# Performance work log

Measured on AMD Instinct MI355X. Metric: run time of the kernel, lower is better.

## Reference

```python
import jax, jax.numpy as jnp
import numpy as np

SHAPE = (192, 192, 192)


def _trilinear_sample(img, z, y, x):
    # img: [B,C,D,H,W]; z,y,x: [B,D,H,W] absolute voxel coords (align_corners=True,
    # zero padding outside the volume, matching F.grid_sample defaults in vroc).
    B, C, D, H, W = img.shape
    imgf = img.reshape(B, C, -1)
    z0 = jnp.floor(z); y0 = jnp.floor(y); x0 = jnp.floor(x)
    wz = z - z0; wy = y - y0; wx = x - x0
    z0i = z0.astype(jnp.int32); y0i = y0.astype(jnp.int32); x0i = x0.astype(jnp.int32)
    z1i = z0i + 1; y1i = y0i + 1; x1i = x0i + 1

    def gather(iz, iy, ix):
        valid = ((iz >= 0) & (iz < D) & (iy >= 0) & (iy < H) & (ix >= 0) & (ix < W))
        lin = ((jnp.clip(iz, 0, D - 1) * H + jnp.clip(iy, 0, H - 1)) * W
               + jnp.clip(ix, 0, W - 1)).reshape(B, 1, -1)
        v = jnp.take_along_axis(imgf, jnp.broadcast_to(lin, (B, C, D * H * W)), axis=2)
        return v.reshape(B, C, D, H, W) * valid.reshape(B, 1, D, H, W).astype(img.dtype)

    def w(a, b, c):
        return (a * b * c)[:, None]  # [B,1,D,H,W]

    out = (gather(z0i, y0i, x0i) * w(1 - wz, 1 - wy, 1 - wx)
           + gather(z0i, y0i, x1i) * w(1 - wz, 1 - wy, wx)
           + gather(z0i, y1i, x0i) * w(1 - wz, wy, 1 - wx)
           + gather(z0i, y1i, x1i) * w(1 - wz, wy, wx)
           + gather(z1i, y0i, x0i) * w(wz, 1 - wy, 1 - wx)
           + gather(z1i, y0i, x1i) * w(wz, 1 - wy, wx)
           + gather(z1i, y1i, x0i) * w(wz, wy, 1 - wx)
           + gather(z1i, y1i, x1i) * w(wz, wy, wx))
    return out


def _warp(moving_image, vector_field):
    # SpatialTransformer: identity grid + displacement (voxel units), trilinear sample.
    B, C, D, H, W = moving_image.shape
    dt = moving_image.dtype
    gz, gy, gx = jnp.meshgrid(jnp.arange(D, dtype=dt), jnp.arange(H, dtype=dt),
                              jnp.arange(W, dtype=dt), indexing='ij')
    z = gz[None] + vector_field[:, 0]
    y = gy[None] + vector_field[:, 1]
    x = gx[None] + vector_field[:, 2]
    return _trilinear_sample(moving_image, z, y, x)


def setup_inputs() -> dict:
    key = jax.random.key(0)
    k1, k2, k3, k4 = jax.random.split(key, 4)
    D, H, W = SHAPE
    moving_image = jax.random.normal(k1, (1, 1, D, H, W), dtype=jnp.float32)
    vector_field = jax.random.normal(k2, (1, 3, D, H, W), dtype=jnp.float32) * 3.0
    fixed_image = jax.random.normal(k3, (1, 1, D, H, W), dtype=jnp.float32)
    fixed_image_mask = jax.random.randint(k4, (1, 1, D, H, W), 0, 2).astype(bool)
    return {"moving_image": moving_image, "vector_field": vector_field,
            "fixed_image": fixed_image, "fixed_image_mask": fixed_image_mask}


def reference(moving_image, vector_field, fixed_image, fixed_image_mask):
    warped = _warp(moving_image, vector_field)
    m = fixed_image_mask.astype(warped.dtype)
    sq = (warped - fixed_image) ** 2
    # F.mse_loss(warped[mask], fixed[mask]) == mean of squared diff over masked voxels
    return jnp.sum(sq * m) / jnp.maximum(jnp.sum(m), 1.0)
```

## Files before the change

### kernel.cpp

```cpp
#include <hip/hip_runtime.h>
#include <hip/hip_fp16.h>

#define DD 192
#define HH 192
#define WW 192
#define NVOX (DD * HH * WW)

#define RSX 32
#define RSY 33
#define RSZ 33
#define ROWD 16
#define SLABD (RSY * ROWD)
#define RTOTH (RSX * RSY * RSZ)
#define RTOTD (RTOTH / 2)
#define NCHUNK (RTOTH / 8)
#define CHSLAB (RSY * 4)
#define NT 1024
#define GRID 256
#define QCAP 512

#define AS1 __attribute__((address_space(1)))
#define AS3 __attribute__((address_space(3)))

__global__ __launch_bounds__(256) void conv_fp16(
    const float4* __restrict__ in, int4* __restrict__ out)
{
    const int i = blockIdx.x * 256 + threadIdx.x;
    const float4 a = in[2 * i];
    const float4 b = in[2 * i + 1];
    __half2 h0 = __floats2half2_rn(a.x, a.y);
    __half2 h1 = __floats2half2_rn(a.z, a.w);
    __half2 h2 = __floats2half2_rn(b.x, b.y);
    __half2 h3 = __floats2half2_rn(b.z, b.w);
    int4 o;
    o.x = *(int*)&h0; o.y = *(int*)&h1; o.z = *(int*)&h2; o.w = *(int*)&h3;
    out[i] = o;
}

struct Streams { float4 dz, dy, dx, f; int4 m; };

__device__ __forceinline__ void tile_coords(int n, int& tx, int& ty, int& tz) {
    tx = n / 144;
    const int r = n - tx * 144;
    ty = r / 12;
    tz = r - ty * 12;
}

__device__ __forceinline__ void stage_tile(
    const ushort* __restrict__ movh, const ushort* __restrict__ zbuf,
    uint* sbufd, int x_lo, int y_lo, int z_lo, int tid)
{
    ushort* sbuf = (ushort*)sbufd;
    #pragma unroll
    for (int i = 0; i < 5; ++i) {
        const int q = tid + i * NT;
        if (q < NCHUNK) {
            const int rz = q / CHSLAB;
            const int rem = q - rz * CHSLAB;
            const int ry = rem >> 2;
            const int k  = rem & 3;
            const int gz = z_lo + rz, gy = y_lo + ry, gx = x_lo + 8 * k;
            const bool valid = ((unsigned)gz < DD) & ((unsigned)gy < HH) &
                               ((unsigned)gx < WW);
            const ushort* src = valid ? (movh + ((gz * HH + gy) * WW + gx)) : zbuf;
            const int qb = i * NT + (tid & ~63);
            __builtin_amdgcn_global_load_lds((AS1 void*)src,
                                             (AS3 void*)(sbuf + 8 * qb), 16, 0, 0);
        }
    }
}

__device__ __forceinline__ Streams prefetch_streams(
    const float* __restrict__ vf, const float* __restrict__ fix,
    const int* __restrict__ mask, int base)
{
    Streams s;
    s.dz = *(const float4*)(vf + base);
    s.dy = *(const float4*)(vf + NVOX + base);
    s.dx = *(const float4*)(vf + 2 * NVOX + base);
    s.f  = *(const float4*)(fix + base);
    s.m  = *(const int4*)(mask + base);
    return s;
}

__global__ __launch_bounds__(NT) void warp_mse_persist(
    const ushort* __restrict__ movh,
    const float* __restrict__ mov,
    const float* __restrict__ vf,
    const float* __restrict__ fix,
    const int* __restrict__ mask,
    const ushort* __restrict__ zbuf,
    float* __restrict__ acc,
    float* __restrict__ out)
{
    __shared__ uint sbufd[2][RTOTD];
    __shared__ float s_sq[16], s_cnt[16];
    __shared__ unsigned qn[2];
    __shared__ uint  qp[QCAP];
    __shared__ float4 qw[QCAP];

    const int tid = threadIdx.x;
    const int b = blockIdx.x;
    const int start = b * 6 + min(b, 192);
    const int cnt_t = 6 + (b < 192 ? 1 : 0);

    const int lxg = (tid & 3) * 4;
    const int ly  = (tid >> 2) & 15;
    const int lz  = tid >> 6;

    float sq = 0.0f, cntm = 0.0f;

    if (tid < 2) qn[tid] = 0;
    int tx, ty, tz;
    tile_coords(start, tx, ty, tz);
    stage_tile(movh, zbuf, sbufd[0], tx * 16 - 8, ty * 16 - 8, tz * 16 - 8, tid);
    Streams S0 = prefetch_streams(vf, fix, mask,
        ((tz * 16 + lz) * HH + ty * 16 + ly) * WW + tx * 16 + lxg);
    __syncthreads();

    for (int k = 0; k < cnt_t; ++k) {
        const int cur = k & 1;
        Streams S1 = S0;
        if (k + 1 < cnt_t) {
            int nx, ny, nz;
            tile_coords(start + k + 1, nx, ny, nz);
            stage_tile(movh, zbuf, sbufd[cur ^ 1],
                       nx * 16 - 8, ny * 16 - 8, nz * 16 - 8, tid);
            S1 = prefetch_streams(vf, fix, mask,
                ((nz * 16 + lz) * HH + ny * 16 + ly) * WW + nx * 16 + lxg);
        }

        int cx, cy, cz;
        tile_coords(start + k, cx, cy, cz);
        const int x_lo = cx * 16 - 8, y_lo = cy * 16 - 8, z_lo = cz * 16 - 8;
        const int gz = cz * 16 + lz, gy = cy * 16 + ly, gx0 = cx * 16 + lxg;
        const uint* sdw = sbufd[cur];

        auto proc = [&](float dz, float dy, float dx, float f, int m, int j) {
            const float z = (float)gz + dz, y = (float)gy + dy,
                        x = (float)(gx0 + j) + dx;
            const float z0f = floorf(z), y0f = floorf(y), x0f = floorf(x);
            const float wz = z - z0f, wy = y - y0f, wx = x - x0f;
            const int z0 = (int)z0f, y0 = (int)y0f, x0 = (int)x0f;
            const int z0l = z0 - z_lo, y0l = y0 - y_lo, x0l = x0 - x_lo;
            const bool inbox = ((unsigned)z0l < RSZ - 1) &
                               ((unsigned)y0l < RSY - 1) &
                               ((unsigned)x0l < RSX - 1);
            if (inbox) {
                const int o = z0l * SLABD + y0l * ROWD + (x0l >> 1);
                const bool odd = (x0l & 1) != 0;
                const uint a00 = sdw[o];
                const uint b00 = sdw[o + 1];
                const uint a01 = sdw[o + ROWD];
                const uint b01 = sdw[o + ROWD + 1];
                const uint a10 = sdw[o + SLABD];
                const uint b10 = sdw[o + SLABD + 1];
                const uint a11 = sdw[o + SLABD + ROWD];
                const uint b11 = sdw[o + SLABD + ROWD + 1];
                float v000, v001, v010, v011, v100, v101, v110, v111;
                auto pr = [&](uint A, uint B, float& l, float& r) {
                    const float2 fa = __half22float2(*(const __half2*)&A);
                    const float fb = __low2float(*(const __half2*)&B);
                    l = odd ? fa.y : fa.x;
                    r = odd ? fb   : fa.y;
                };
                pr(a00, b00, v000, v001);
                pr(a01, b01, v010, v011);
                pr(a10, b10, v100, v101);
                pr(a11, b11, v110, v111);
                const float c00 = v000 + (v001 - v000) * wx;
                const float c01 = v010 + (v011 - v010) * wx;
                const float c10 = v100 + (v101 - v100) * wx;
                const float c11 = v110 + (v111 - v110) * wx;
                const float c0 = c00 + (c01 - c00) * wy;
                const float c1 = c10 + (c11 - c10) * wy;
                const float warped = c0 + (c1 - c0) * wz;
                const float mm = (m != 0) ? 1.0f : 0.0f;
                const float diff = warped - f;
                sq += diff * diff * mm;
                cntm += mm;
            } else {
                const uint slot = atomicAdd(&qn[cur], 1u);
                if (slot < QCAP) {
                    const int px = min(max(x0, -5), 196) + 8;
                    const int py = min(max(y0, -5), 196) + 8;
                    const int pz = min(max(z0, -5), 196) + 8;
                    qp[slot] = (uint)px | ((uint)py << 8) | ((uint)pz << 16) |
                               ((m != 0) ? 0x80000000u : 0u);
                    qw[slot] = make_float4(wx, wy, wz, f);
                } else {
                    const int z1 = z0 + 1, y1 = y0 + 1, x1 = x0 + 1;
                    const bool zi0 = (unsigned)z0 < DD, zi1 = (unsigned)z1 < DD;
                    const bool yi0 = (unsigned)y0 < HH, yi1 = (unsigned)y1 < HH;
                    const bool xi0 = (unsigned)x0 < WW, xi1 = (unsigned)x1 < WW;
                    auto ld = [&](int iz, int iy, int ix, bool ok) -> float {
                        return ok ? mov[(iz * HH + iy) * WW + ix] : 0.0f;
                    };
                    const float v000 = ld(z0, y0, x0, zi0 & yi0 & xi0);
                    const float v001 = ld(z0, y0, x1, zi0 & yi0 & xi1);
                    const float v010 = ld(z0, y1, x0, zi0 & yi1 & xi0);
                    const float v011 = ld(z0, y1, x1, zi0 & yi1 & xi1);
                    const float v100 = ld(z1, y0, x0, zi1 & yi0 & xi0);
                    const float v101 = ld(z1, y0, x1, zi1 & yi0 & xi1);
                    const float v110 = ld(z1, y1, x0, zi1 & yi1 & xi0);
                    const float v111 = ld(z1, y1, x1, zi1 & yi1 & xi1);
                    const float c00 = v000 + (v001 - v000) * wx;
                    const float c01 = v010 + (v011 - v010) * wx;
                    const float c10 = v100 + (v101 - v100) * wx;
                    const float c11 = v110 + (v111 - v110) * wx;
                    const float c0 = c00 + (c01 - c00) * wy;
                    const float c1 = c10 + (c11 - c10) * wy;
                    const float warped = c0 + (c1 - c0) * wz;
                    const float mm = (m != 0) ? 1.0f : 0.0f;
                    const float diff = warped - f;
                    sq += diff * diff * mm;
                    cntm += mm;
                }
            }
        };
        proc(S0.dz.x, S0.dy.x, S0.dx.x, S0.f.x, S0.m.x, 0);
        proc(S0.dz.y, S0.dy.y, S0.dx.y, S0.f.y, S0.m.y, 1);
        proc(S0.dz.z, S0.dy.z, S0.dx.z, S0.f.z, S0.m.z, 2);
        proc(S0.dz.w, S0.dy.w, S0.dx.w, S0.f.w, S0.m.w, 3);

        __syncthreads();

        const uint qcount = min(qn[cur], (uint)QCAP);
        if (tid == 0) qn[cur ^ 1] = 0;
        for (uint i = tid; i < qcount; i += NT) {
            const uint pos = qp[i];
            const float4 w4 = qw[i];
            const int x0 = (int)(pos & 255u) - 8;
            const int y0 = (int)((pos >> 8) & 255u) - 8;
            const int z0 = (int)((pos >> 16) & 255u) - 8;
            const float mm = (pos & 0x80000000u) ? 1.0f : 0.0f;
            const int z1 = z0 + 1, y1 = y0 + 1, x1 = x0 + 1;
            const bool zi0 = (unsigned)z0 < DD, zi1 = (unsigned)z1 < DD;
            const bool yi0 = (unsigned)y0 < HH, yi1 = (unsigned)y1 < HH;
            const bool xi0 = (unsigned)x0 < WW, xi1 = (unsigned)x1 < WW;
            auto ld = [&](int iz, int iy, int ix, bool ok) -> float {
                return ok ? __half2float(*(const __half*)(movh +
                                ((iz * HH + iy) * WW + ix))) : 0.0f;
            };
            const float v000 = ld(z0, y0, x0, zi0 & yi0 & xi0);
            const float v001 = ld(z0, y0, x1, zi0 & yi0 & xi1);
            const float v010 = ld(z0, y1, x0, zi0 & yi1 & xi0);
            const float v011 = ld(z0, y1, x1, zi0 & yi1 & xi1);
            const float v100 = ld(z1, y0, x0, zi1 & yi0 & xi0);
            const float v101 = ld(z1, y0, x1, zi1 & yi0 & xi1);
            const float v110 = ld(z1, y1, x0, zi1 & yi1 & xi0);
            const float v111 = ld(z1, y1, x1, zi1 & yi1 & xi1);
            const float wx = w4.x, wy = w4.y, wz = w4.z;
            const float c00 = v000 + (v001 - v000) * wx;
            const float c01 = v010 + (v011 - v010) * wx;
            const float c10 = v100 + (v101 - v100) * wx;
            const float c11 = v110 + (v111 - v110) * wx;
            const float c0 = c00 + (c01 - c00) * wy;
            const float c1 = c10 + (c11 - c10) * wy;
            const float warped = c0 + (c1 - c0) * wz;
            const float diff = warped - w4.w;
            sq += diff * diff * mm;
            cntm += mm;
        }

        __syncthreads();
        S0 = S1;
    }

    #pragma unroll
    for (int off = 32; off > 0; off >>= 1) {
        sq   += __shfl_down(sq, off, 64);
        cntm += __shfl_down(cntm, off, 64);
    }
    const int lane = tid & 63;
    const int wid = tid >> 6;
    if (lane == 0) { s_sq[wid] = sq; s_cnt[wid] = cntm; }
    __syncthreads();
    if (tid == 0) {
        float bsq = 0.0f, bcnt = 0.0f;
        #pragma unroll
        for (int i = 0; i < 16; ++i) { bsq += s_sq[i]; bcnt += s_cnt[i]; }
        atomicAdd(&acc[0], bsq);
        atomicAdd(&acc[1], bcnt);
        __threadfence();
        const unsigned old = atomicAdd((unsigned*)&acc[2], 1u);
        if (old == GRID - 1) {
            __threadfence();
            const float s = atomicAdd(&acc[0], 0.0f);
            const float c = atomicAdd(&acc[1], 0.0f);
            out[0] = s / fmaxf(c, 1.0f);
        }
    }
}

__global__ __launch_bounds__(256) void warp_mse_simple(
    const float* __restrict__ mov, const float* __restrict__ vf,
    const float* __restrict__ fix, const int* __restrict__ mask,
    float* __restrict__ acc)
{
    const int idx = blockIdx.x * 256 + threadIdx.x;
    float sq = 0.0f, cnt = 0.0f;
    if (idx < NVOX) {
        const int w = idx % WW;
        const int t = idx / WW;
        const int h = t % HH;
        const int d = t / HH;
        const float z = (float)d + vf[idx];
        const float y = (float)h + vf[NVOX + idx];
        const float x = (float)w + vf[2 * NVOX + idx];
        const float z0f = floorf(z), y0f = floorf(y), x0f = floorf(x);
        const float wz = z - z0f, wy = y - y0f, wx = x - x0f;
        const int z0 = (int)z0f, y0 = (int)y0f, x0 = (int)x0f;
        const int z1 = z0 + 1, y1 = y0 + 1, x1 = x0 + 1;
        const bool zi0 = (unsigned)z0 < DD, zi1 = (unsigned)z1 < DD;
        const bool yi0 = (unsigned)y0 < HH, yi1 = (unsigned)y1 < HH;
        const bool xi0 = (unsigned)x0 < WW, xi1 = (unsigned)x1 < WW;
        auto ld = [&](int iz, int iy, int ix, bool ok) -> float {
            return ok ? mov[(iz * HH + iy) * WW + ix] : 0.0f;
        };
        const float v000 = ld(z0, y0, x0, zi0 & yi0 & xi0);
        const float v001 = ld(z0, y0, x1, zi0 & yi0 & xi1);
        const float v010 = ld(z0, y1, x0, zi0 & yi1 & xi0);
        const float v011 = ld(z0, y1, x1, zi0 & yi1 & xi1);
        const float v100 = ld(z1, y0, x0, zi1 & yi0 & xi0);
        const float v101 = ld(z1, y0, x1, zi1 & yi0 & xi1);
        const float v110 = ld(z1, y1, x0, zi1 & yi1 & xi0);
        const float v111 = ld(z1, y1, x1, zi1 & yi1 & xi1);
        const float c00 = v000 + (v001 - v000) * wx;
        const float c01 = v010 + (v011 - v010) * wx;
        const float c10 = v100 + (v101 - v100) * wx;
        const float c11 = v110 + (v111 - v110) * wx;
        const float c0 = c00 + (c01 - c00) * wy;
        const float c1 = c10 + (c11 - c10) * wy;
        const float warped = c0 + (c1 - c0) * wz;
        const float m = (mask[idx] != 0) ? 1.0f : 0.0f;
        const float diff = warped - fix[idx];
        sq = diff * diff * m;
        cnt = m;
    }
    #pragma unroll
    for (int off = 32; off > 0; off >>= 1) {
        sq  += __shfl_down(sq, off, 64);
        cnt += __shfl_down(cnt, off, 64);
    }
    __shared__ float s_sq[4], s_cnt[4];
    const int lane = threadIdx.x & 63, wid = threadIdx.x >> 6;
    if (lane == 0) { s_sq[wid] = sq; s_cnt[wid] = cnt; }
    __syncthreads();
    if (threadIdx.x == 0) {
        atomicAdd(&acc[0], s_sq[0] + s_sq[1] + s_sq[2] + s_sq[3]);
        atomicAdd(&acc[1], s_cnt[0] + s_cnt[1] + s_cnt[2] + s_cnt[3]);
    }
}

__global__ void warp_mse_finalize(const float* __restrict__ acc, float* __restrict__ out) {
    out[0] = acc[0] / fmaxf(acc[1], 1.0f);
}

extern "C" void kernel_launch(void* const* d_in, const int* in_sizes, int n_in,
                              void* d_out, int out_size, void* d_ws, size_t ws_size,
                              hipStream_t stream) {
    const float* mov  = (const float*)d_in[0];
    const float* vf   = (const float*)d_in[1];
    const float* fix  = (const float*)d_in[2];
    const int*   mask = (const int*)d_in[3];
    float* acc = (float*)d_ws;
    float* out = (float*)d_out;

    hipMemsetAsync(d_ws, 0, 256, stream);

    const size_t need = 256 + (size_t)NVOX * 2;
    if (ws_size >= need) {
        ushort* movh = (ushort*)((char*)d_ws + 256);
        const ushort* zbuf = (const ushort*)((char*)d_ws + 64);
        conv_fp16<<<NVOX / (256 * 8), 256, 0, stream>>>(
            (const float4*)mov, (int4*)movh);
        warp_mse_persist<<<GRID, NT, 0, stream>>>(movh, mov, vf, fix, mask,
                                                  zbuf, acc, out);
    } else {
        warp_mse_simple<<<(NVOX + 255) / 256, 256, 0, stream>>>(mov, vf, fix, mask, acc);
        warp_mse_finalize<<<1, 1, 0, stream>>>(acc, out);
    }
}
```

Baseline: 249.4 us.

## Replace per-tile halo staging with z-sliding ring buffer of fp16 slabs

```diff
diff --git a/kernel.cpp b/kernel.cpp
--- a/kernel.cpp
+++ b/kernel.cpp
@@ -6,18 +6,20 @@
 #define WW 192
 #define NVOX (DD * HH * WW)
 
-#define RSX 32
-#define RSY 33
-#define RSZ 33
-#define ROWD 16
-#define SLABD (RSY * ROWD)
-#define RTOTH (RSX * RSY * RSZ)
-#define RTOTD (RTOTH / 2)
-#define NCHUNK (RTOTH / 8)
-#define CHSLAB (RSY * 4)
+#define ROWH 32
+#define ROWDW 16
+#define NROWS 29
+#define SLABH (NROWS * ROWH)
+#define SLABDW (SLABH / 2)
+#define RING 32
+#define RINGDW (RING * SLABDW)
+#define CHPS (NROWS * 4)
+#define TILEZ 8
+#define ZSEG 48
+#define NSTEP (ZSEG / TILEZ)
 #define NT 1024
-#define GRID 256
-#define QCAP 512
+#define NBLK (12 * 12 * 4)
+#define QCAP 128
 
 #define AS1 __attribute__((address_space(1)))
 #define AS3 __attribute__((address_space(3)))
@@ -37,36 +39,25 @@
     out[i] = o;
 }
 
-struct Streams { float4 dz, dy, dx, f; int4 m; };
-
-__device__ __forceinline__ void tile_coords(int n, int& tx, int& ty, int& tz) {
-    tx = n / 144;
-    const int r = n - tx * 144;
-    ty = r / 12;
-    tz = r - ty * 12;
-}
-
-__device__ __forceinline__ void stage_tile(
+struct Streams { float2 dz, dy, dx, f; int2 m; };
+
+__device__ __forceinline__ void stage8(
     const ushort* __restrict__ movh, const ushort* __restrict__ zbuf,
-    uint* sbufd, int x_lo, int y_lo, int z_lo, int tid)
-{
-    ushort* sbuf = (ushort*)sbufd;
-    #pragma unroll
-    for (int i = 0; i < 5; ++i) {
-        const int q = tid + i * NT;
-        if (q < NCHUNK) {
-            const int rz = q / CHSLAB;
-            const int rem = q - rz * CHSLAB;
-            const int ry = rem >> 2;
-            const int k  = rem & 3;
-            const int gz = z_lo + rz, gy = y_lo + ry, gx = x_lo + 8 * k;
-            const bool valid = ((unsigned)gz < DD) & ((unsigned)gy < HH) &
-                               ((unsigned)gx < WW);
-            const ushort* src = valid ? (movh + ((gz * HH + gy) * WW + gx)) : zbuf;
-            const int qb = i * NT + (tid & ~63);
-            __builtin_amdgcn_global_load_lds((AS1 void*)src,
-                                             (AS3 void*)(sbuf + 8 * qb), 16, 0, 0);
-        }
+    ushort* ring, int x_lo, int y_lo, int zfirst, int zlim, int tid)
+{
+    const int wave = tid >> 6, lane = tid & 63;
+    const int z = zfirst + (wave >> 1);
+    const int part = wave & 1;
+    const int c = part * 64 + lane;
+    if (z < zlim && c < CHPS) {
+        const int row = c >> 2, k = c & 3;
+        const int gy = y_lo + row, gx = x_lo + 8 * k;
+        const bool valid = ((unsigned)z < DD) & ((unsigned)gy < HH) &
+                           ((unsigned)gx < WW);
+        const ushort* src = valid ? (movh + ((z * HH + gy) * WW + gx)) : zbuf;
+        const int baseh = (z & 31) * SLABH + part * 512;
+        __builtin_amdgcn_global_load_lds((AS1 void*)src,
+                                         (AS3 void*)(ring + baseh), 16, 0, 0);
     }
 }
 
@@ -75,15 +66,15 @@
     const int* __restrict__ mask, int base)
 {
     Streams s;
-    s.dz = *(const float4*)(vf + base);
-    s.dy = *(const float4*)(vf + NVOX + base);
-    s.dx = *(const float4*)(vf + 2 * NVOX + base);
-    s.f  = *(const float4*)(fix + base);
-    s.m  = *(const int4*)(mask + base);
+    s.dz = *(const float2*)(vf + base);
+    s.dy = *(const float2*)(vf + NVOX + base);
+    s.dx = *(const float2*)(vf + 2 * NVOX + base);
+    s.f  = *(const float2*)(fix + base);
+    s.m  = *(const int2*)(mask + base);
     return s;
 }
 
-__global__ __launch_bounds__(NT) void warp_mse_persist(
+__global__ __launch_bounds__(NT) void warp_mse_ring(
     const ushort* __restrict__ movh,
     const float* __restrict__ mov,
     const float* __restrict__ vf,
@@ -93,7 +84,7 @@
     float* __restrict__ acc,
     float* __restrict__ out)
 {
-    __shared__ uint sbufd[2][RTOTD];
+    __shared__ ushort ring[RING * SLABH + 16];
     __shared__ float s_sq[16], s_cnt[16];
     __shared__ unsigned qn[2];
     __shared__ uint  qp[QCAP];
@@ -101,40 +92,41 @@
 
     const int tid = threadIdx.x;
     const int b = blockIdx.x;
-    const int start = b * 6 + min(b, 192);
-    const int cnt_t = 6 + (b < 192 ? 1 : 0);
-
-    const int lxg = (tid & 3) * 4;
-    const int ly  = (tid >> 2) & 15;
-    const int lz  = tid >> 6;
+    const int cx = b % 12;
+    const int cy = (b / 12) % 12;
+    const int s  = (b / 144) * ZSEG;
+    const int bx0 = cx * 16, by0 = cy * 16;
+    const int x_lo = bx0 - 8, y_lo = by0 - 6;
+
+    const int lxp = (tid & 7) * 2;
+    const int ly  = (tid >> 3) & 15;
+    const int lz  = tid >> 7;
+    const int gy = by0 + ly, gx0 = bx0 + lxp;
 
     float sq = 0.0f, cntm = 0.0f;
 
     if (tid < 2) qn[tid] = 0;
-    int tx, ty, tz;
-    tile_coords(start, tx, ty, tz);
-    stage_tile(movh, zbuf, sbufd[0], tx * 16 - 8, ty * 16 - 8, tz * 16 - 8, tid);
+    stage8(movh, zbuf, ring, x_lo, y_lo, s - 6,      s + 15, tid);
+    stage8(movh, zbuf, ring, x_lo, y_lo, s + 2,      s + 15, tid);
+    stage8(movh, zbuf, ring, x_lo, y_lo, s + 10,     s + 15, tid);
     Streams S0 = prefetch_streams(vf, fix, mask,
-        ((tz * 16 + lz) * HH + ty * 16 + ly) * WW + tx * 16 + lxg);
+        (((s + lz) * HH + gy) * WW + gx0));
     __syncthreads();
 
-    for (int k = 0; k < cnt_t; ++k) {
+    const uint* sdw = (const uint*)ring;
+
+    for (int k = 0; k < NSTEP; ++k) {
+        const int t = s + k * TILEZ;
         const int cur = k & 1;
         Streams S1 = S0;
-        if (k + 1 < cnt_t) {
-            int nx, ny, nz;
-            tile_coords(start + k + 1, nx, ny, nz);
-            stage_tile(movh, zbuf, sbufd[cur ^ 1],
-                       nx * 16 - 8, ny * 16 - 8, nz * 16 - 8, tid);
+        if (k + 1 < NSTEP) {
+            stage8(movh, zbuf, ring, x_lo, y_lo, t + 15, t + 23, tid);
             S1 = prefetch_streams(vf, fix, mask,
-                ((nz * 16 + lz) * HH + ny * 16 + ly) * WW + nx * 16 + lxg);
+                (((t + TILEZ + lz) * HH + gy) * WW + gx0));
         }
 
-        int cx, cy, cz;
-        tile_coords(start + k, cx, cy, cz);
-        const int x_lo = cx * 16 - 8, y_lo = cy * 16 - 8, z_lo = cz * 16 - 8;
-        const int gz = cz * 16 + lz, gy = cy * 16 + ly, gx0 = cx * 16 + lxg;
-        const uint* sdw = sbufd[cur];
+        const int gz = t + lz;
+        const int zlo_t = t - 6;
 
         auto proc = [&](float dz, float dy, float dx, float f, int m, int j) {
             const float z = (float)gz + dz, y = (float)gy + dy,
@@ -142,21 +134,22 @@
             const float z0f = floorf(z), y0f = floorf(y), x0f = floorf(x);
             const float wz = z - z0f, wy = y - y0f, wx = x - x0f;
             const int z0 = (int)z0f, y0 = (int)y0f, x0 = (int)x0f;
-            const int z0l = z0 - z_lo, y0l = y0 - y_lo, x0l = x0 - x_lo;
-            const bool inbox = ((unsigned)z0l < RSZ - 1) &
-                               ((unsigned)y0l < RSY - 1) &
-                               ((unsigned)x0l < RSX - 1);
+            const int z0l = z0 - zlo_t, y0l = y0 - y_lo, x0l = x0 - x_lo;
+            const bool inbox = ((unsigned)z0l < 20u) & ((unsigned)y0l < 28u) &
+                               ((unsigned)x0l < 31u);
             if (inbox) {
-                const int o = z0l * SLABD + y0l * ROWD + (x0l >> 1);
+                const int col = x0l >> 1;
                 const bool odd = (x0l & 1) != 0;
-                const uint a00 = sdw[o];
-                const uint b00 = sdw[o + 1];
-                const uint a01 = sdw[o + ROWD];
-                const uint b01 = sdw[o + ROWD + 1];
-                const uint a10 = sdw[o + SLABD];
-                const uint b10 = sdw[o + SLABD + 1];
-                const uint a11 = sdw[o + SLABD + ROWD];
-                const uint b11 = sdw[o + SLABD + ROWD + 1];
+                const int o0 = (z0 & 31) * SLABDW + y0l * ROWDW + col;
+                const int o1 = ((z0 + 1) & 31) * SLABDW + y0l * ROWDW + col;
+                const uint a00 = sdw[o0];
+                const uint b00 = sdw[o0 + 1];
+                const uint a01 = sdw[o0 + ROWDW];
+                const uint b01 = sdw[o0 + ROWDW + 1];
+                const uint a10 = sdw[o1];
+                const uint b10 = sdw[o1 + 1];
+                const uint a11 = sdw[o1 + ROWDW];
+                const uint b11 = sdw[o1 + ROWDW + 1];
                 float v000, v001, v010, v011, v100, v101, v110, v111;
                 auto pr = [&](uint A, uint B, float& l, float& r) {
                     const float2 fa = __half22float2(*(const __half2*)&A);
@@ -194,7 +187,8 @@
                     const bool yi0 = (unsigned)y0 < HH, yi1 = (unsigned)y1 < HH;
                     const bool xi0 = (unsigned)x0 < WW, xi1 = (unsigned)x1 < WW;
                     auto ld = [&](int iz, int iy, int ix, bool ok) -> float {
-                        return ok ? mov[(iz * HH + iy) * WW + ix] : 0.0f;
+                        return ok ? __half2float(*(const __half*)(movh +
+                                        ((iz * HH + iy) * WW + ix))) : 0.0f;
                     };
                     const float v000 = ld(z0, y0, x0, zi0 & yi0 & xi0);
                     const float v001 = ld(z0, y0, x1, zi0 & yi0 & xi1);
@@ -220,8 +214,6 @@
         };
         proc(S0.dz.x, S0.dy.x, S0.dx.x, S0.f.x, S0.m.x, 0);
         proc(S0.dz.y, S0.dy.y, S0.dx.y, S0.f.y, S0.m.y, 1);
-        proc(S0.dz.z, S0.dy.z, S0.dx.z, S0.f.z, S0.m.z, 2);
-        proc(S0.dz.w, S0.dy.w, S0.dx.w, S0.f.w, S0.m.w, 3);
 
         __syncthreads();
 
@@ -284,11 +276,11 @@
         atomicAdd(&acc[1], bcnt);
         __threadfence();
         const unsigned old = atomicAdd((unsigned*)&acc[2], 1u);
-        if (old == GRID - 1) {
+        if (old == NBLK - 1) {
             __threadfence();
-            const float s = atomicAdd(&acc[0], 0.0f);
-            const float c = atomicAdd(&acc[1], 0.0f);
-            out[0] = s / fmaxf(c, 1.0f);
+            const float s2 = atomicAdd(&acc[0], 0.0f);
+            const float c2 = atomicAdd(&acc[1], 0.0f);
+            out[0] = s2 / fmaxf(c2, 1.0f);
         }
     }
 }
@@ -375,8 +367,8 @@
         const ushort* zbuf = (const ushort*)((char*)d_ws + 64);
         conv_fp16<<<NVOX / (256 * 8), 256, 0, stream>>>(
             (const float4*)mov, (int4*)movh);
-        warp_mse_persist<<<GRID, NT, 0, stream>>>(movh, mov, vf, fix, mask,
-                                                  zbuf, acc, out);
+        warp_mse_ring<<<NBLK, NT, 0, stream>>>(movh, mov, vf, fix, mask,
+                                               zbuf, acc, out);
     } else {
         warp_mse_simple<<<(NVOX + 255) / 256, 256, 0, stream>>>(mov, vf, fix, mask, acc);
         warp_mse_finalize<<<1, 1, 0, stream>>>(acc, out);
```

New measurement: 258.6 us. +3.7%, slower.
